# Kernel optimization log

Hardware: AMD Instinct MI355X
Metric: run time of the kernel (lower is better)

## Reference

```python
import jax, jax.numpy as jnp
import numpy as np

SCALE, Z, X, Y = 4, 9, 9, 9
INV_SQRT_2PI = 1.0 / np.sqrt(2.0 * np.pi)


def setup_inputs() -> dict:
    key = jax.random.key(0)
    k1, = jax.random.split(key, 1)
    inp = jax.random.normal(k1, (1, 1, 128, 512, 512), dtype=jnp.float32)
    return {
        "inp": inp,
        "mu_z": jnp.asarray(0.0, dtype=jnp.float32),
        "sig_z": jnp.asarray(0.1, dtype=jnp.float32),
        "bet_xy": jnp.asarray(2.0, dtype=jnp.float32),
        "bet_z": jnp.asarray(1.5, dtype=jnp.float32),
    }


def _gen_alf(bet_xy, bet_z):
    # squared distances along each axis; torch's loop overwrites the wrap-around
    # write, so the net result for odd sizes is simply (arange - size//2)**2
    zd = ((jnp.arange(Z) - Z // 2) ** 2).astype(jnp.float32)[:, None, None]
    xd = ((jnp.arange(X) - X // 2) ** 2).astype(jnp.float32)[None, :, None]
    yd = ((jnp.arange(Y) - Y // 2) ** 2).astype(jnp.float32)[None, None, :]
    d_2 = zd / bet_z ** 2 + (xd + yd) / bet_xy ** 2  # (Z, X, Y)
    return jnp.exp(-d_2 / 2) * INV_SQRT_2PI


def reference(inp, mu_z, sig_z, bet_xy, bet_z):
    z0 = jnp.exp(mu_z + 0.5 * sig_z ** 2)
    rec = inp * z0  # (N, 1, D, H, W)
    alf = _gen_alf(bet_xy, bet_z)[None, None]  # (1, 1, Z, X, Y)
    pad_z = (Z - SCALE + 1) // 2
    rec = jax.lax.conv_general_dilated(
        rec, alf,
        window_strides=(SCALE, 1, 1),
        padding=[(pad_z, pad_z), (X // 2, X // 2), (Y // 2, Y // 2)],
        dimension_numbers=("NCDHW", "OIDHW", "NCDHW"),
    )  # (N, 1, D//SCALE, H, W)
    rec = (rec - rec.min()) / (rec.max() - rec.min())
    return rec
```

## Files before the change

### kernel.cpp

```cpp
#include <hip/hip_runtime.h>

#define D_IN  128
#define D_OUT 32
#define H     512
#define W     512
#define W4    128
#define HB    8
#define ZR    (HB + 8)
#define K2THR 512

__device__ __forceinline__ unsigned f2key(float f) {
    unsigned u = __float_as_uint(f);
    return (u & 0x80000000u) ? ~u : (u | 0x80000000u);
}
__device__ __forceinline__ float key2f(unsigned k) {
    unsigned u = (k & 0x80000000u) ? (k ^ 0x80000000u) : ~k;
    return __uint_as_float(u);
}

__global__ void zconv_kernel(const float* __restrict__ inp, float* __restrict__ out,
                             const float* __restrict__ bz_p, unsigned* __restrict__ fin_u) {
    if (blockIdx.x == 0 && threadIdx.x == 0) {
        fin_u[0] = 0xFFFFFFFFu;
        fin_u[1] = 0u;
    }
    int tid = blockIdx.x * blockDim.x + threadIdx.x;
    int w4 = tid & (W4 - 1);
    int h  = (tid >> 7) & (H - 1);
    int d  = tid >> 16;
    float bz = bz_p[0];
    float iz = 1.0f / (2.0f * bz * bz);
    float wz[9];
#pragma unroll
    for (int k = 0; k < 9; ++k) {
        float dd = (float)(k - 4);
        wz[k] = expf(-dd * dd * iz);
    }
    const float4* in4 = (const float4*)inp;
    float4 acc = make_float4(0.f, 0.f, 0.f, 0.f);
    int base = h * W4 + w4;
#pragma unroll
    for (int k = 0; k < 9; ++k) {
        int din = 4 * d - 3 + k;
        if ((unsigned)din < D_IN) {
            float4 v = in4[din * (H * W4) + base];
            acc.x += v.x * wz[k]; acc.y += v.y * wz[k];
            acc.z += v.z * wz[k]; acc.w += v.w * wz[k];
        }
    }
    ((float4*)out)[d * (H * W4) + base] = acc;
}

__global__ __launch_bounds__(K2THR)
void hwconv_kernel(const float* __restrict__ in, float* __restrict__ out,
                   const float* __restrict__ bxy_p, unsigned* __restrict__ fin_u) {
    __shared__ float zbuf[ZR * W];
    __shared__ float hbuf[HB * W];
    __shared__ float smin[8], smax[8];

    const int d  = blockIdx.x >> 6;
    const int h0 = (blockIdx.x & 63) * HB;

    float bx = bxy_p[0];
    float ix = 1.0f / (2.0f * bx * bx);
    float wx[9];
#pragma unroll
    for (int k = 0; k < 9; ++k) {
        float dd = (float)(k - 4);
        wx[k] = expf(-dd * dd * ix);
    }

    const float4* in4 = (const float4*)in;
    float4* z4 = (float4*)zbuf;
    float4* h4 = (float4*)hbuf;

#pragma unroll
    for (int i = 0; i < (ZR * W4) / K2THR; ++i) {
        int t  = threadIdx.x + i * K2THR;
        int r  = t >> 7;
        int c4 = t & (W4 - 1);
        int h  = h0 - 4 + r;
        z4[t] = ((unsigned)h < H) ? in4[(d * H + h) * W4 + c4]
                                  : make_float4(0.f, 0.f, 0.f, 0.f);
    }
    __syncthreads();

#pragma unroll
    for (int i = 0; i < (HB * W4) / K2THR; ++i) {
        int t  = threadIdx.x + i * K2THR;
        int r  = t >> 7;
        int c4 = t & (W4 - 1);
        float4 acc = make_float4(0.f, 0.f, 0.f, 0.f);
#pragma unroll
        for (int k = 0; k < 9; ++k) {
            float4 v = z4[(r + k) * W4 + c4];
            acc.x += v.x * wx[k]; acc.y += v.y * wx[k];
            acc.z += v.z * wx[k]; acc.w += v.w * wx[k];
        }
        h4[t] = acc;
    }
    __syncthreads();

    float lmin =  3.402823466e38f;
    float lmax = -3.402823466e38f;
    float4* out4 = (float4*)out;
#pragma unroll
    for (int i = 0; i < (HB * W4) / K2THR; ++i) {
        int t  = threadIdx.x + i * K2THR;
        int r  = t >> 7;
        int c4 = t & (W4 - 1);
        float4 zv = make_float4(0.f, 0.f, 0.f, 0.f);
        float4 va = (c4 > 0)      ? h4[r * W4 + c4 - 1] : zv;
        float4 vb =                 h4[r * W4 + c4];
        float4 vc = (c4 < W4 - 1) ? h4[r * W4 + c4 + 1] : zv;
        float win[12] = {va.x, va.y, va.z, va.w,
                         vb.x, vb.y, vb.z, vb.w,
                         vc.x, vc.y, vc.z, vc.w};
        float4 o = make_float4(0.f, 0.f, 0.f, 0.f);
#pragma unroll
        for (int k = 0; k < 9; ++k) {
            o.x += win[k]     * wx[k];
            o.y += win[k + 1] * wx[k];
            o.z += win[k + 2] * wx[k];
            o.w += win[k + 3] * wx[k];
        }
        out4[(d * H + h0 + r) * W4 + c4] = o;
        lmin = fminf(lmin, fminf(fminf(o.x, o.y), fminf(o.z, o.w)));
        lmax = fmaxf(lmax, fmaxf(fmaxf(o.x, o.y), fmaxf(o.z, o.w)));
    }

#pragma unroll
    for (int off = 32; off > 0; off >>= 1) {
        lmin = fminf(lmin, __shfl_down(lmin, off, 64));
        lmax = fmaxf(lmax, __shfl_down(lmax, off, 64));
    }
    int lane = threadIdx.x & 63, wv = threadIdx.x >> 6;
    if (lane == 0) { smin[wv] = lmin; smax[wv] = lmax; }
    __syncthreads();
    if (threadIdx.x == 0) {
        float mn = smin[0], mx = smax[0];
#pragma unroll
        for (int i = 1; i < 8; ++i) { mn = fminf(mn, smin[i]); mx = fmaxf(mx, smax[i]); }
        atomicMin(&fin_u[0], f2key(mn));
        atomicMax(&fin_u[1], f2key(mx));
    }
}

__global__ void norm_kernel(const float* __restrict__ in, float* __restrict__ out,
                            const unsigned* __restrict__ fin_u) {
    int tid = blockIdx.x * blockDim.x + threadIdx.x;
    float mn  = key2f(fin_u[0]);
    float mx  = key2f(fin_u[1]);
    float inv = 1.0f / (mx - mn);
    float4 v = ((const float4*)in)[tid];
    ((float4*)out)[tid] = make_float4((v.x - mn) * inv, (v.y - mn) * inv,
                                      (v.z - mn) * inv, (v.w - mn) * inv);
}

extern "C" void kernel_launch(void* const* d_in, const int* in_sizes, int n_in,
                              void* d_out, int out_size, void* d_ws, size_t ws_size,
                              hipStream_t stream) {
    const float* inp    = (const float*)d_in[0];
    const float* bet_xy = (const float*)d_in[3];
    const float* bet_z  = (const float*)d_in[4];
    float* out = (float*)d_out;

    char* ws = (char*)d_ws;
    unsigned* fin_u = (unsigned*)ws;
    float* bufA = (float*)(ws + 65536);
    float* bufB = (float*)(ws + 65536 + (size_t)33554432);

    const int NTASK = D_OUT * H * W4;
    zconv_kernel<<<NTASK / 256, 256, 0, stream>>>(inp, bufA, bet_z, fin_u);
    hwconv_kernel<<<D_OUT * (H / HB), K2THR, 0, stream>>>(bufA, bufB, bet_xy, fin_u);
    norm_kernel<<<NTASK / 256, 256, 0, stream>>>(bufB, out, fin_u);
}
```

Baseline: 269.4 us.

## Fuse z-conv, hw-conv and normalize into one cooperative persistent kernel

Merges the three separate launches (z convolution, separable h/w convolution with min/max, normalization) into a single persistent cooperative kernel that uses grid-wide syncs between phases. Grid size comes from occupancy queries and is capped at the number of tiles. The aim is to remove launch gaps and the kernel-boundary tails between phases. In exchange it adds grid-sync costs, and with 48KB of shared memory per block the occupancy and grid size may be lower than with separate launches, while intermediate buffers still round-trip through global memory.

Result: slower. 350.5 us (+30.1%).

```diff
diff --git a/kernel.cpp b/kernel.cpp
--- a/kernel.cpp
+++ b/kernel.cpp
@@ -1,4 +1,8 @@
 #include <hip/hip_runtime.h>
+#include <hip/hip_cooperative_groups.h>
+#include <float.h>
+
+namespace cg = cooperative_groups;
 
 #define D_IN  128
 #define D_OUT 32
@@ -7,7 +11,9 @@
 #define W4    128
 #define HB    8
 #define ZR    (HB + 8)
-#define K2THR 512
+#define NTHR  512
+#define NTILE (D_OUT * (H / HB))
+#define NT    (D_OUT * H * W4)
 
 __device__ __forceinline__ unsigned f2key(float f) {
     unsigned u = __float_as_uint(f);
@@ -18,115 +24,109 @@
     return __uint_as_float(u);
 }
 
-__global__ void zconv_kernel(const float* __restrict__ inp, float* __restrict__ out,
-                             const float* __restrict__ bz_p, unsigned* __restrict__ fin_u) {
+__global__ __launch_bounds__(NTHR)
+void fused_all(const float* __restrict__ inp, float* __restrict__ bufA,
+               float* __restrict__ bufB, float* __restrict__ out,
+               const float* __restrict__ bxy_p, const float* __restrict__ bz_p,
+               unsigned* __restrict__ fin_u) {
+    cg::grid_group grid = cg::this_grid();
+    __shared__ float zbuf[ZR * W];
+    __shared__ float hbuf[HB * W];
+    __shared__ float smin[8], smax[8];
+
     if (blockIdx.x == 0 && threadIdx.x == 0) {
         fin_u[0] = 0xFFFFFFFFu;
         fin_u[1] = 0u;
     }
-    int tid = blockIdx.x * blockDim.x + threadIdx.x;
-    int w4 = tid & (W4 - 1);
-    int h  = (tid >> 7) & (H - 1);
-    int d  = tid >> 16;
-    float bz = bz_p[0];
-    float iz = 1.0f / (2.0f * bz * bz);
-    float wz[9];
+
+    const float bz = bz_p[0], bx = bxy_p[0];
+    const float iz = 1.0f / (2.0f * bz * bz);
+    const float ix = 1.0f / (2.0f * bx * bx);
+    float wz[9], wx[9];
 #pragma unroll
     for (int k = 0; k < 9; ++k) {
         float dd = (float)(k - 4);
         wz[k] = expf(-dd * dd * iz);
-    }
-    const float4* in4 = (const float4*)inp;
-    float4 acc = make_float4(0.f, 0.f, 0.f, 0.f);
-    int base = h * W4 + w4;
-#pragma unroll
-    for (int k = 0; k < 9; ++k) {
-        int din = 4 * d - 3 + k;
-        if ((unsigned)din < D_IN) {
-            float4 v = in4[din * (H * W4) + base];
-            acc.x += v.x * wz[k]; acc.y += v.y * wz[k];
-            acc.z += v.z * wz[k]; acc.w += v.w * wz[k];
-        }
-    }
-    ((float4*)out)[d * (H * W4) + base] = acc;
-}
-
-__global__ __launch_bounds__(K2THR)
-void hwconv_kernel(const float* __restrict__ in, float* __restrict__ out,
-                   const float* __restrict__ bxy_p, unsigned* __restrict__ fin_u) {
-    __shared__ float zbuf[ZR * W];
-    __shared__ float hbuf[HB * W];
-    __shared__ float smin[8], smax[8];
-
-    const int d  = blockIdx.x >> 6;
-    const int h0 = (blockIdx.x & 63) * HB;
-
-    float bx = bxy_p[0];
-    float ix = 1.0f / (2.0f * bx * bx);
-    float wx[9];
-#pragma unroll
-    for (int k = 0; k < 9; ++k) {
-        float dd = (float)(k - 4);
         wx[k] = expf(-dd * dd * ix);
     }
 
-    const float4* in4 = (const float4*)in;
+    const float4* in4 = (const float4*)inp;
+    float4* a4 = (float4*)bufA;
+    float4* b4 = (float4*)bufB;
+    float4* o4 = (float4*)out;
     float4* z4 = (float4*)zbuf;
     float4* h4 = (float4*)hbuf;
 
-#pragma unroll
-    for (int i = 0; i < (ZR * W4) / K2THR; ++i) {
-        int t  = threadIdx.x + i * K2THR;
-        int r  = t >> 7;
-        int c4 = t & (W4 - 1);
-        int h  = h0 - 4 + r;
-        z4[t] = ((unsigned)h < H) ? in4[(d * H + h) * W4 + c4]
-                                  : make_float4(0.f, 0.f, 0.f, 0.f);
-    }
-    __syncthreads();
+    const int gstr = gridDim.x * NTHR;
 
-#pragma unroll
-    for (int i = 0; i < (HB * W4) / K2THR; ++i) {
-        int t  = threadIdx.x + i * K2THR;
-        int r  = t >> 7;
-        int c4 = t & (W4 - 1);
+    for (int t = blockIdx.x * NTHR + threadIdx.x; t < NT; t += gstr) {
+        int base = t & 0xFFFF;
+        int d    = t >> 16;
         float4 acc = make_float4(0.f, 0.f, 0.f, 0.f);
 #pragma unroll
         for (int k = 0; k < 9; ++k) {
-            float4 v = z4[(r + k) * W4 + c4];
-            acc.x += v.x * wx[k]; acc.y += v.y * wx[k];
-            acc.z += v.z * wx[k]; acc.w += v.w * wx[k];
+            int din = 4 * d - 3 + k;
+            if ((unsigned)din < D_IN) {
+                float4 v = in4[din * (H * W4) + base];
+                acc.x += v.x * wz[k]; acc.y += v.y * wz[k];
+                acc.z += v.z * wz[k]; acc.w += v.w * wz[k];
+            }
         }
-        h4[t] = acc;
+        a4[t] = acc;
     }
-    __syncthreads();
+    grid.sync();
 
-    float lmin =  3.402823466e38f;
-    float lmax = -3.402823466e38f;
-    float4* out4 = (float4*)out;
+    float lmin = FLT_MAX, lmax = -FLT_MAX;
+    for (int tile = blockIdx.x; tile < NTILE; tile += gridDim.x) {
+        const int d  = tile >> 6;
+        const int h0 = (tile & 63) * HB;
 #pragma unroll
-    for (int i = 0; i < (HB * W4) / K2THR; ++i) {
-        int t  = threadIdx.x + i * K2THR;
-        int r  = t >> 7;
-        int c4 = t & (W4 - 1);
-        float4 zv = make_float4(0.f, 0.f, 0.f, 0.f);
-        float4 va = (c4 > 0)      ? h4[r * W4 + c4 - 1] : zv;
-        float4 vb =                 h4[r * W4 + c4];
-        float4 vc = (c4 < W4 - 1) ? h4[r * W4 + c4 + 1] : zv;
-        float win[12] = {va.x, va.y, va.z, va.w,
-                         vb.x, vb.y, vb.z, vb.w,
-                         vc.x, vc.y, vc.z, vc.w};
-        float4 o = make_float4(0.f, 0.f, 0.f, 0.f);
+        for (int i = 0; i < (ZR * W4) / NTHR; ++i) {
+            int t = threadIdx.x + i * NTHR;
+            int r = t >> 7, c4 = t & (W4 - 1);
+            int h = h0 - 4 + r;
+            z4[t] = ((unsigned)h < H) ? a4[(d * H + h) * W4 + c4]
+                                      : make_float4(0.f, 0.f, 0.f, 0.f);
+        }
+        __syncthreads();
 #pragma unroll
-        for (int k = 0; k < 9; ++k) {
-            o.x += win[k]     * wx[k];
-            o.y += win[k + 1] * wx[k];
-            o.z += win[k + 2] * wx[k];
-            o.w += win[k + 3] * wx[k];
+        for (int i = 0; i < (HB * W4) / NTHR; ++i) {
+            int t = threadIdx.x + i * NTHR;
+            int r = t >> 7, c4 = t & (W4 - 1);
+            float4 acc = make_float4(0.f, 0.f, 0.f, 0.f);
+#pragma unroll
+            for (int k = 0; k < 9; ++k) {
+                float4 v = z4[(r + k) * W4 + c4];
+                acc.x += v.x * wx[k]; acc.y += v.y * wx[k];
+                acc.z += v.z * wx[k]; acc.w += v.w * wx[k];
+            }
+            h4[t] = acc;
         }
-        out4[(d * H + h0 + r) * W4 + c4] = o;
-        lmin = fminf(lmin, fminf(fminf(o.x, o.y), fminf(o.z, o.w)));
-        lmax = fmaxf(lmax, fmaxf(fmaxf(o.x, o.y), fmaxf(o.z, o.w)));
+        __syncthreads();
+#pragma unroll
+        for (int i = 0; i < (HB * W4) / NTHR; ++i) {
+            int t = threadIdx.x + i * NTHR;
+            int r = t >> 7, c4 = t & (W4 - 1);
+            float4 zv = make_float4(0.f, 0.f, 0.f, 0.f);
+            float4 va = (c4 > 0)      ? h4[r * W4 + c4 - 1] : zv;
+            float4 vb =                 h4[r * W4 + c4];
+            float4 vc = (c4 < W4 - 1) ? h4[r * W4 + c4 + 1] : zv;
+            float win[12] = {va.x, va.y, va.z, va.w,
+                             vb.x, vb.y, vb.z, vb.w,
+                             vc.x, vc.y, vc.z, vc.w};
+            float4 o = make_float4(0.f, 0.f, 0.f, 0.f);
+#pragma unroll
+            for (int k = 0; k < 9; ++k) {
+                o.x += win[k]     * wx[k];
+                o.y += win[k + 1] * wx[k];
+                o.z += win[k + 2] * wx[k];
+                o.w += win[k + 3] * wx[k];
+            }
+            b4[(d * H + h0 + r) * W4 + c4] = o;
+            lmin = fminf(lmin, fminf(fminf(o.x, o.y), fminf(o.z, o.w)));
+            lmax = fmaxf(lmax, fmaxf(fmaxf(o.x, o.y), fmaxf(o.z, o.w)));
+        }
+        __syncthreads();
     }
 
 #pragma unroll
@@ -144,17 +144,15 @@
         atomicMin(&fin_u[0], f2key(mn));
         atomicMax(&fin_u[1], f2key(mx));
     }
-}
+    grid.sync();
 
-__global__ void norm_kernel(const float* __restrict__ in, float* __restrict__ out,
-                            const unsigned* __restrict__ fin_u) {
-    int tid = blockIdx.x * blockDim.x + threadIdx.x;
     float mn  = key2f(fin_u[0]);
-    float mx  = key2f(fin_u[1]);
-    float inv = 1.0f / (mx - mn);
-    float4 v = ((const float4*)in)[tid];
-    ((float4*)out)[tid] = make_float4((v.x - mn) * inv, (v.y - mn) * inv,
-                                      (v.z - mn) * inv, (v.w - mn) * inv);
+    float inv = 1.0f / (key2f(fin_u[1]) - mn);
+    for (int t = blockIdx.x * NTHR + threadIdx.x; t < NT; t += gstr) {
+        float4 v = b4[t];
+        o4[t] = make_float4((v.x - mn) * inv, (v.y - mn) * inv,
+                            (v.z - mn) * inv, (v.w - mn) * inv);
+    }
 }
 
 extern "C" void kernel_launch(void* const* d_in, const int* in_sizes, int n_in,
@@ -170,8 +168,19 @@
     float* bufA = (float*)(ws + 65536);
     float* bufB = (float*)(ws + 65536 + (size_t)33554432);
 
-    const int NTASK = D_OUT * H * W4;
-    zconv_kernel<<<NTASK / 256, 256, 0, stream>>>(inp, bufA, bet_z, fin_u);
-    hwconv_kernel<<<D_OUT * (H / HB), K2THR, 0, stream>>>(bufA, bufB, bet_xy, fin_u);
-    norm_kernel<<<NTASK / 256, 256, 0, stream>>>(bufB, out, fin_u);
+    static int grid_blocks = [] {
+        int per_cu = 0;
+        hipOccupancyMaxActiveBlocksPerMultiprocessor(&per_cu, fused_all, NTHR, 0);
+        if (per_cu < 1) per_cu = 1;
+        hipDeviceProp_t p;
+        int cus = 256;
+        if (hipGetDeviceProperties(&p, 0) == hipSuccess) cus = p.multiProcessorCount;
+        int g = per_cu * cus;
+        return g > NTILE ? NTILE : g;
+    }();
+
+    void* args[] = {(void*)&inp, (void*)&bufA, (void*)&bufB, (void*)&out,
+                    (void*)&bet_xy, (void*)&bet_z, (void*)&fin_u};
+    hipLaunchCooperativeKernel((const void*)fused_all, dim3(grid_blocks), dim3(NTHR),
+                               args, 0, stream);
 }
```

## Fuse depth convolution into the spatial convolution tile kernel

Applied to the files above, without the earlier changes.

The separate depth-axis convolution kernel is folded into the tiled H/W convolution kernel. Each block now computes the strided 9-tap depth convolution straight from the input into its shared-memory row buffer, so the 32 MB intermediate buffer is never written or read back. Because each 8-row tile needs 16 rows including the halo, the depth convolution and its input reads are done twice per output row, leaning on cache to absorb the extra traffic. The min/max accumulator reset moves out of the kernel into two small async memsets.

Result: faster. 262.7 us (-2.5%).

```diff
diff --git a/kernel.cpp b/kernel.cpp
--- a/kernel.cpp
+++ b/kernel.cpp
@@ -1,4 +1,5 @@
 #include <hip/hip_runtime.h>
+#include <float.h>
 
 #define D_IN  128
 #define D_OUT 32
@@ -7,7 +8,8 @@
 #define W4    128
 #define HB    8
 #define ZR    (HB + 8)
-#define K2THR 512
+#define NTHR  512
+#define NTILE (D_OUT * (H / HB))
 
 __device__ __forceinline__ unsigned f2key(float f) {
     unsigned u = __float_as_uint(f);
@@ -18,42 +20,10 @@
     return __uint_as_float(u);
 }
 
-__global__ void zconv_kernel(const float* __restrict__ inp, float* __restrict__ out,
-                             const float* __restrict__ bz_p, unsigned* __restrict__ fin_u) {
-    if (blockIdx.x == 0 && threadIdx.x == 0) {
-        fin_u[0] = 0xFFFFFFFFu;
-        fin_u[1] = 0u;
-    }
-    int tid = blockIdx.x * blockDim.x + threadIdx.x;
-    int w4 = tid & (W4 - 1);
-    int h  = (tid >> 7) & (H - 1);
-    int d  = tid >> 16;
-    float bz = bz_p[0];
-    float iz = 1.0f / (2.0f * bz * bz);
-    float wz[9];
-#pragma unroll
-    for (int k = 0; k < 9; ++k) {
-        float dd = (float)(k - 4);
-        wz[k] = expf(-dd * dd * iz);
-    }
-    const float4* in4 = (const float4*)inp;
-    float4 acc = make_float4(0.f, 0.f, 0.f, 0.f);
-    int base = h * W4 + w4;
-#pragma unroll
-    for (int k = 0; k < 9; ++k) {
-        int din = 4 * d - 3 + k;
-        if ((unsigned)din < D_IN) {
-            float4 v = in4[din * (H * W4) + base];
-            acc.x += v.x * wz[k]; acc.y += v.y * wz[k];
-            acc.z += v.z * wz[k]; acc.w += v.w * wz[k];
-        }
-    }
-    ((float4*)out)[d * (H * W4) + base] = acc;
-}
-
-__global__ __launch_bounds__(K2THR)
-void hwconv_kernel(const float* __restrict__ in, float* __restrict__ out,
-                   const float* __restrict__ bxy_p, unsigned* __restrict__ fin_u) {
+__global__ __launch_bounds__(NTHR)
+void conv3d_fused(const float* __restrict__ inp, float* __restrict__ out,
+                  const float* __restrict__ bxy_p, const float* __restrict__ bz_p,
+                  unsigned* __restrict__ fin_u) {
     __shared__ float zbuf[ZR * W];
     __shared__ float hbuf[HB * W];
     __shared__ float smin[8], smax[8];
@@ -61,33 +31,47 @@
     const int d  = blockIdx.x >> 6;
     const int h0 = (blockIdx.x & 63) * HB;
 
-    float bx = bxy_p[0];
-    float ix = 1.0f / (2.0f * bx * bx);
-    float wx[9];
+    const float bz = bz_p[0], bx = bxy_p[0];
+    const float iz = 1.0f / (2.0f * bz * bz);
+    const float ix = 1.0f / (2.0f * bx * bx);
+    float wz[9], wx[9];
 #pragma unroll
     for (int k = 0; k < 9; ++k) {
         float dd = (float)(k - 4);
+        wz[k] = expf(-dd * dd * iz);
         wx[k] = expf(-dd * dd * ix);
     }
 
-    const float4* in4 = (const float4*)in;
+    const float4* in4 = (const float4*)inp;
     float4* z4 = (float4*)zbuf;
     float4* h4 = (float4*)hbuf;
 
 #pragma unroll
-    for (int i = 0; i < (ZR * W4) / K2THR; ++i) {
-        int t  = threadIdx.x + i * K2THR;
+    for (int i = 0; i < (ZR * W4) / NTHR; ++i) {
+        int t  = threadIdx.x + i * NTHR;
         int r  = t >> 7;
         int c4 = t & (W4 - 1);
         int h  = h0 - 4 + r;
-        z4[t] = ((unsigned)h < H) ? in4[(d * H + h) * W4 + c4]
-                                  : make_float4(0.f, 0.f, 0.f, 0.f);
+        float4 acc = make_float4(0.f, 0.f, 0.f, 0.f);
+        if ((unsigned)h < H) {
+            int base = h * W4 + c4;
+#pragma unroll
+            for (int k = 0; k < 9; ++k) {
+                int din = 4 * d - 3 + k;
+                if ((unsigned)din < D_IN) {
+                    float4 v = in4[din * (H * W4) + base];
+                    acc.x += v.x * wz[k]; acc.y += v.y * wz[k];
+                    acc.z += v.z * wz[k]; acc.w += v.w * wz[k];
+                }
+            }
+        }
+        z4[t] = acc;
     }
     __syncthreads();
 
 #pragma unroll
-    for (int i = 0; i < (HB * W4) / K2THR; ++i) {
-        int t  = threadIdx.x + i * K2THR;
+    for (int i = 0; i < (HB * W4) / NTHR; ++i) {
+        int t  = threadIdx.x + i * NTHR;
         int r  = t >> 7;
         int c4 = t & (W4 - 1);
         float4 acc = make_float4(0.f, 0.f, 0.f, 0.f);
@@ -101,12 +85,11 @@
     }
     __syncthreads();
 
-    float lmin =  3.402823466e38f;
-    float lmax = -3.402823466e38f;
+    float lmin = FLT_MAX, lmax = -FLT_MAX;
     float4* out4 = (float4*)out;
 #pragma unroll
-    for (int i = 0; i < (HB * W4) / K2THR; ++i) {
-        int t  = threadIdx.x + i * K2THR;
+    for (int i = 0; i < (HB * W4) / NTHR; ++i) {
+        int t  = threadIdx.x + i * NTHR;
         int r  = t >> 7;
         int c4 = t & (W4 - 1);
         float4 zv = make_float4(0.f, 0.f, 0.f, 0.f);
@@ -150,8 +133,7 @@
                             const unsigned* __restrict__ fin_u) {
     int tid = blockIdx.x * blockDim.x + threadIdx.x;
     float mn  = key2f(fin_u[0]);
-    float mx  = key2f(fin_u[1]);
-    float inv = 1.0f / (mx - mn);
+    float inv = 1.0f / (key2f(fin_u[1]) - mn);
     float4 v = ((const float4*)in)[tid];
     ((float4*)out)[tid] = make_float4((v.x - mn) * inv, (v.y - mn) * inv,
                                       (v.z - mn) * inv, (v.w - mn) * inv);
@@ -167,11 +149,13 @@
 
     char* ws = (char*)d_ws;
     unsigned* fin_u = (unsigned*)ws;
-    float* bufA = (float*)(ws + 65536);
-    float* bufB = (float*)(ws + 65536 + (size_t)33554432);
+    float* bufB = (float*)(ws + 65536);
+
+    hipMemsetAsync(&fin_u[0], 0xFF, 4, stream);
+    hipMemsetAsync(&fin_u[1], 0x00, 4, stream);
+
+    conv3d_fused<<<NTILE, NTHR, 0, stream>>>(inp, bufB, bet_xy, bet_z, fin_u);
 
     const int NTASK = D_OUT * H * W4;
-    zconv_kernel<<<NTASK / 256, 256, 0, stream>>>(inp, bufA, bet_z, fin_u);
-    hwconv_kernel<<<D_OUT * (H / HB), K2THR, 0, stream>>>(bufA, bufB, bet_xy, fin_u);
     norm_kernel<<<NTASK / 256, 256, 0, stream>>>(bufB, out, fin_u);
 }
```
